# Performance work log

Measured on AMD Instinct MI355X. Metric: run time of the kernel, lower is better.

Reference implementation:

```python
import jax, jax.numpy as jnp
import numpy as np

D_MODEL = 1024
NUM_HEADS = 16
HEAD_DIM = D_MODEL // NUM_HEADS
ROPE_THETA = 10000.0


def apply_rope(x):
    # x: (B, H, S, d_k) interleaved-pair RoPE, angles pos / theta^(2i/d_k)
    S, d_k = x.shape[-2], x.shape[-1]
    inv_freq = ROPE_THETA ** (jnp.arange(0, d_k, 2, dtype=jnp.float32) / d_k)
    ang = jnp.arange(S, dtype=jnp.float32)[:, None] / inv_freq[None, :]  # (S, d_k/2)
    cos, sin = jnp.cos(ang), jnp.sin(ang)
    xp = x.reshape(x.shape[:-1] + (d_k // 2, 2))
    x0, x1 = xp[..., 0], xp[..., 1]
    out = jnp.stack([x0 * cos - x1 * sin, x0 * sin + x1 * cos], axis=-1)
    return out.reshape(x.shape)


def setup_inputs() -> dict:
    key = jax.random.key(0)
    k1, k2, k3 = jax.random.split(key, 3)
    B, S = 2, 2048
    std = 2.0 / (D_MODEL + 3 * D_MODEL)
    std_o = 2.0 / (D_MODEL + D_MODEL)
    return {
        "x": jax.random.normal(k1, (B, S, D_MODEL), dtype=jnp.float32),
        "W_qkv": jax.random.normal(k2, (3 * D_MODEL, D_MODEL), dtype=jnp.float32) * std,
        "W_o": jax.random.normal(k3, (D_MODEL, D_MODEL), dtype=jnp.float32) * std_o,
    }


def reference(x, W_qkv, W_o):
    B, S, d_model = x.shape
    H, d_k = NUM_HEADS, HEAD_DIM
    qkv = jnp.einsum('bsi,oi->bso', x, W_qkv)  # (B, S, 3*d_model)
    Q, K, V = jnp.split(qkv, 3, axis=-1)
    # (B, S, d_model) -> (B, H, S, d_k)
    def to_heads(t):
        return t.reshape(B, S, H, d_k).transpose(0, 2, 1, 3)
    Q, K, V = to_heads(Q), to_heads(K), to_heads(V)
    Q, K = apply_rope(Q), apply_rope(K)
    scores = jnp.einsum('bhqd,bhkd->bhqk', Q, K) / jnp.sqrt(jnp.float32(d_k))
    causal = jnp.tril(jnp.ones((S, S), dtype=bool))
    scores = jnp.where(causal, scores, -jnp.inf)
    attn = jax.nn.softmax(scores, axis=-1)
    out = jnp.einsum('bhqk,bhkd->bhqd', attn, V)
    out = out.transpose(0, 2, 1, 3).reshape(B, S, d_model)
    return jnp.einsum('bsi,oi->bso', out, W_o)
```

## Files before the change

kernel.cpp:

```cpp
#include <hip/hip_runtime.h>
#include <math.h>

#define kB 2
#define kS 2048
#define kD 1024
#define kH 16
#define kDk 64
#define kM (kB * kS)
#define kNT (kD / 64)
#define kLog2Theta 13.287712379549449
#define C_SCALE 0.18033688011112042f

typedef __attribute__((ext_vector_type(4))) float f32x4;
typedef __attribute__((ext_vector_type(16))) float f32x16;
typedef __attribute__((ext_vector_type(8))) __bf16 bf16x8;

__device__ __forceinline__ ushort f2bf(float f) {
  uint u = __float_as_uint(f);
  return (ushort)((u + 0x7fffu + ((u >> 16) & 1u)) >> 16);
}
__device__ __forceinline__ uint cvt_pk_bf16(float lo, float hi) {
  uint r;
  asm("v_cvt_pk_bf16_f32 %0, %1, %2" : "=v"(r) : "v"(lo), "v"(hi));
  return r;
}

typedef __attribute__((address_space(1))) void gvoid;
typedef __attribute__((address_space(3))) void lvoid;
__device__ __forceinline__ void load_lds16(const void* g, void* l) {
  __builtin_amdgcn_global_load_lds((gvoid*)g, (lvoid*)l, 16, 0, 0);
}

__global__ __launch_bounds__(256) void rope_table_kernel(float2* __restrict__ tab) {
  const int i = blockIdx.x * 256 + threadIdx.x;
  const int s = i >> 5, p = i & 31;
  const double ang = (double)s * exp2(-(double)p * (kLog2Theta / 32.0));
  tab[i] = make_float2((float)cos(ang), (float)sin(ang));
}

__global__ __launch_bounds__(256) void cast_all_kernel(
    const float* __restrict__ x, const float* __restrict__ wq,
    const float* __restrict__ wo, ushort* __restrict__ xb,
    ushort* __restrict__ wqb, ushort* __restrict__ wob) {
  const int i = blockIdx.x * 256 + threadIdx.x;
  const float* src;
  ushort* dst;
  int off;
  if (i < 1048576) {
    src = x; dst = xb; off = i;
  } else if (i < 1048576 + 786432) {
    src = wq; dst = wqb; off = i - 1048576;
  } else {
    src = wo; dst = wob; off = i - 1835008;
  }
  const float4 v = reinterpret_cast<const float4*>(src)[off];
  ushort4 o;
  o.x = f2bf(v.x); o.y = f2bf(v.y); o.z = f2bf(v.z); o.w = f2bf(v.w);
  reinterpret_cast<ushort4*>(dst)[off] = o;
}

__global__ __launch_bounds__(512) void qkv_mfma_kernel(
    const ushort* __restrict__ xb, const ushort* __restrict__ wqb,
    const float2* __restrict__ tab,
    ushort* __restrict__ q, ushort* __restrict__ k, ushort* __restrict__ vt) {
  __shared__ ushort As0[256 * 64], Bs0[256 * 64];
  __shared__ ushort As1[256 * 64], Bs1[256 * 64];
  const int tid = threadIdx.x;
  const int lane = tid & 63;
  const int wid = tid >> 6;
  const int wmi = wid >> 2, wni = wid & 3;
  const int fr = lane & 15, fq = lane >> 4;

  const int bid = blockIdx.x;
  const int xcd = bid & 7, li = bid >> 3;
  const int mt = ((xcd >> 1) << 2) + (li & 3);
  const int ntl = (xcd & 1) * 6 + (li >> 2);
  const int m0 = mt << 8, n0 = ntl << 8;

  f32x4 acc[8][4];
#pragma unroll
  for (int i = 0; i < 8; ++i)
#pragma unroll
    for (int j = 0; j < 4; ++j) acc[i][j] = {0.f, 0.f, 0.f, 0.f};

  auto stage = [&](int k0, ushort* Ad, ushort* Bd) {
#pragma unroll
    for (int u = 0; u < 4; ++u) {
      const int c = u * 512 + tid;
      const int r = c >> 3, sl = c & 7;
      const int col = k0 + ((sl ^ (r & 7)) << 3);
      load_lds16(&xb[(size_t)(m0 + r) * kD + col], &Ad[c << 3]);
      load_lds16(&wqb[(size_t)(n0 + r) * kD + col], &Bd[c << 3]);
    }
  };
  auto rdfrag = [&](const ushort* S, int row, int kk) -> bf16x8 {
    const int off = ((kk << 5) + (fq << 3)) ^ ((row & 7) << 3);
    return *reinterpret_cast<const bf16x8*>(&S[(row << 6) + off]);
  };

  stage(0, As0, Bs0);

  auto tile = [&](const ushort* cA, const ushort* cB, ushort* nA, ushort* nB,
                  bool pf, int k0n) {
    asm volatile("s_waitcnt vmcnt(0)" ::: "memory");
    __builtin_amdgcn_s_barrier();
    __builtin_amdgcn_sched_barrier(0);
#pragma unroll
    for (int kk = 0; kk < 2; ++kk) {
      bf16x8 af[8], bf_[4];
#pragma unroll
      for (int f = 0; f < 8; ++f)
        af[f] = rdfrag(cA, (wmi << 7) + f * 16 + fr, kk);
#pragma unroll
      for (int f = 0; f < 4; ++f)
        bf_[f] = rdfrag(cB, (wni << 6) + f * 16 + fr, kk);
      if (kk == 0 && pf) stage(k0n, nA, nB);
      asm volatile("s_waitcnt lgkmcnt(0)" ::: "memory");
      __builtin_amdgcn_sched_barrier(0);
      __builtin_amdgcn_s_setprio(1);
#pragma unroll
      for (int i = 0; i < 8; ++i)
#pragma unroll
        for (int j = 0; j < 4; ++j)
          acc[i][j] = __builtin_amdgcn_mfma_f32_16x16x32_bf16(
              af[i], bf_[j], acc[i][j], 0, 0, 0);
      __builtin_amdgcn_s_setprio(0);
    }
  };

  for (int t = 0; t < kNT; t += 2) {
    tile(As0, Bs0, As1, Bs1, true, (t + 1) << 6);
    tile(As1, Bs1, As0, Bs0, t + 2 < kNT, (t + 2) << 6);
  }

  const int tsel = n0 >> 10;
#pragma unroll
  for (int i = 0; i < 8; ++i) {
    const int mbase = m0 + (wmi << 7) + i * 16 + fq * 4;
    const int b = mbase >> 11, sbase = mbase & (kS - 1);
#pragma unroll
    for (int j = 0; j < 4; ++j) {
      const int n = n0 + (wni << 6) + j * 16 + fr;
      const int h = (n >> 6) & 15, d = n & 63;
      if (tsel == 2) {
        ushort4 o;
        o.x = f2bf(acc[i][j][0]);
        o.y = f2bf(acc[i][j][1]);
        o.z = f2bf(acc[i][j][2]);
        o.w = f2bf(acc[i][j][3]);
        *reinterpret_cast<ushort4*>(
            &vt[(((size_t)((b << 4) + h) << 6) + d) * kS + sbase]) = o;
      } else {
        ushort* dst = (tsel == 0) ? q : k;
#pragma unroll
        for (int r = 0; r < 4; ++r) {
          const int s = sbase + r;
          float val = acc[i][j][r];
          const float2 cs = tab[(s << 5) + (d >> 1)];
          const float partner = __shfl_xor(val, 1);
          val = (d & 1) ? (partner * cs.y + val * cs.x)
                        : (val * cs.x - partner * cs.y);
          if (tsel == 0) val *= C_SCALE;
          dst[(((size_t)((b << 4) + h) << 11) + s) * kDk + d] = f2bf(val);
        }
      }
    }
  }
}

__global__ __launch_bounds__(256) void proj_mfma_kernel(
    const ushort* __restrict__ ab, const ushort* __restrict__ wob,
    float* __restrict__ out) {
  __shared__ ushort As0[128 * 64], Bs0[128 * 64];
  __shared__ ushort As1[128 * 64], Bs1[128 * 64];
  const int tid = threadIdx.x;
  const int lane = tid & 63;
  const int wid = tid >> 6;
  const int wm = (wid >> 1) << 6, wn = (wid & 1) << 6;
  const int fr = lane & 15, fq = lane >> 4;

  const int bid = blockIdx.x;
  const int xcd = bid & 7, li = bid >> 3;
  const int mt = ((xcd >> 1) << 3) + (li & 7);
  const int ntl = ((xcd & 1) << 2) + (li >> 3);
  const int m0 = mt << 7, n0 = ntl << 7;

  f32x4 acc[4][4];
#pragma unroll
  for (int i = 0; i < 4; ++i)
#pragma unroll
    for (int j = 0; j < 4; ++j) acc[i][j] = {0.f, 0.f, 0.f, 0.f};

  auto stage = [&](int k0, ushort* Ad, ushort* Bd) {
#pragma unroll
    for (int u = 0; u < 4; ++u) {
      const int c = u * 256 + tid;
      const int r = c >> 3, sl = c & 7;
      const int col = k0 + ((sl ^ (r & 7)) << 3);
      load_lds16(&ab[(size_t)(m0 + r) * kD + col], &Ad[c << 3]);
      load_lds16(&wob[(size_t)(n0 + r) * kD + col], &Bd[c << 3]);
    }
  };
  auto rdfrag = [&](const ushort* S, int row, int kk) -> bf16x8 {
    const int off = ((kk << 5) + (fq << 3)) ^ ((row & 7) << 3);
    return *reinterpret_cast<const bf16x8*>(&S[(row << 6) + off]);
  };

  stage(0, As0, Bs0);

  auto tile = [&](const ushort* cA, const ushort* cB, ushort* nA, ushort* nB,
                  bool pf, int k0n) {
    asm volatile("s_waitcnt vmcnt(0)" ::: "memory");
    __builtin_amdgcn_s_barrier();
    __builtin_amdgcn_sched_barrier(0);
    bf16x8 af[2][4], bf_[2][4];
#pragma unroll
    for (int kk = 0; kk < 2; ++kk)
#pragma unroll
      for (int f = 0; f < 4; ++f) {
        af[kk][f]  = rdfrag(cA, wm + f * 16 + fr, kk);
        bf_[kk][f] = rdfrag(cB, wn + f * 16 + fr, kk);
      }
    if (pf) stage(k0n, nA, nB);
    asm volatile("s_waitcnt lgkmcnt(0)" ::: "memory");
    __builtin_amdgcn_sched_barrier(0);
    __builtin_amdgcn_s_setprio(1);
#pragma unroll
    for (int kk = 0; kk < 2; ++kk)
#pragma unroll
      for (int i = 0; i < 4; ++i)
#pragma unroll
        for (int j = 0; j < 4; ++j)
          acc[i][j] = __builtin_amdgcn_mfma_f32_16x16x32_bf16(
              af[kk][i], bf_[kk][j], acc[i][j], 0, 0, 0);
    __builtin_amdgcn_s_setprio(0);
  };

  for (int t = 0; t < kNT; t += 2) {
    tile(As0, Bs0, As1, Bs1, true, (t + 1) << 6);
    tile(As1, Bs1, As0, Bs0, t + 2 < kNT, (t + 2) << 6);
  }

#pragma unroll
  for (int i = 0; i < 4; ++i)
#pragma unroll
    for (int j = 0; j < 4; ++j)
#pragma unroll
      for (int r = 0; r < 4; ++r)
        out[(size_t)(m0 + wm + i * 16 + fq * 4 + r) * kD + n0 + wn + j * 16 + fr] =
            acc[i][j][r];
}

__global__ __launch_bounds__(256) void attn_mfma_kernel(
    const ushort* __restrict__ q, const ushort* __restrict__ k,
    const ushort* __restrict__ vt, ushort* __restrict__ ob) {
  __shared__ ushort smem[32768];
  const int tid = threadIdx.x;
  const int lane = tid & 63;
  const int wq = tid >> 6;
  const int l5 = lane >> 5;
  const int ln = lane & 31;
  const int swz = (ln & 7) << 4;

  const int bidx = blockIdx.x;
  const int xcd = bidx & 7, li = bidx >> 3;
  const int bh = (xcd << 2) + (li & 3);
  const int grp = li >> 2;
  const int qi = (grp < 8) ? (15 - grp) : (grp - 8);
  const int qb = qi << 7;
  const int nt = qi + 1;

  const ushort* qp = q + (size_t)bh * kS * kDk;
  const ushort* kp = k + (size_t)bh * kS * kDk;
  const ushort* vp = vt + (size_t)bh * kDk * kS;

  bf16x8 bq[4];
#pragma unroll
  for (int kk = 0; kk < 4; ++kk)
    bq[kk] = *reinterpret_cast<const bf16x8*>(
        &qp[(size_t)(qb + wq * 32 + ln) * kDk + kk * 16 + l5 * 8]);

  f32x16 acc_o[2];
#pragma unroll
  for (int db = 0; db < 2; ++db)
#pragma unroll
    for (int r = 0; r < 16; ++r) acc_o[db][r] = 0.f;
  float l_run = 0.f;

  auto stage = [&](int kt, int buf) {
    ushort* Kd = smem + buf * 16384;
    ushort* Vd = Kd + 8192;
#pragma unroll
    for (int u = 0; u < 4; ++u) {
      const int c = u * 256 + tid;
      {
        const int r = c >> 3, sl = c & 7;
        load_lds16(&kp[(size_t)(kt * 128 + r) * kDk + ((sl ^ (r & 7)) << 3)],
                   &Kd[c << 3]);
      }
      {
        const int r = c >> 4, sl = c & 15;
        load_lds16(&vp[(size_t)r * kS + kt * 128 + ((sl ^ (r & 7)) << 3)],
                   &Vd[c << 3]);
      }
    }
  };

  stage(0, 0);

  for (int kt = 0; kt < nt; ++kt) {
    const int cur = kt & 1;
    __syncthreads();
    if (kt + 1 < nt) stage(kt + 1, cur ^ 1);

    const char* KsB = reinterpret_cast<const char*>(smem + cur * 16384);
    const char* VtsB = KsB + 16384;

    f32x16 accs[4];
    __builtin_amdgcn_s_setprio(1);
#pragma unroll
    for (int cb = 0; cb < 4; ++cb) {
#pragma unroll
      for (int r = 0; r < 16; ++r) accs[cb][r] = 0.f;
#pragma unroll
      for (int kk = 0; kk < 4; ++kk) {
        const bf16x8 av = *reinterpret_cast<const bf16x8*>(
            KsB + (cb * 32 + ln) * 128 + ((kk * 32 + l5 * 16) ^ swz));
        accs[cb] = __builtin_amdgcn_mfma_f32_32x32x16_bf16(av, bq[kk], accs[cb], 0, 0, 0);
      }
    }
    __builtin_amdgcn_s_setprio(0);

    if (kt == qi) {
      const int lim = (wq << 5) + ln;
#pragma unroll
      for (int cb = 0; cb < 4; ++cb)
#pragma unroll
        for (int r = 0; r < 16; ++r) {
          const int key = cb * 32 + (r & 3) + 8 * (r >> 2) + 4 * l5;
          if (key > lim) accs[cb][r] = -INFINITY;
        }
    }

    uint c8[4][8];
    float lsum = 0.f;
#pragma unroll
    for (int cb = 0; cb < 4; ++cb) {
      float s0 = 0.f, s1 = 0.f, s2 = 0.f, s3 = 0.f;
      float p[16];
#pragma unroll
      for (int r = 0; r < 16; ++r) {
        p[r] = exp2f(accs[cb][r]);
        if ((r & 3) == 0) s0 += p[r];
        else if ((r & 3) == 1) s1 += p[r];
        else if ((r & 3) == 2) s2 += p[r];
        else s3 += p[r];
      }
      lsum += (s0 + s1) + (s2 + s3);
#pragma unroll
      for (int t = 0; t < 8; ++t)
        c8[cb][t] = cvt_pk_bf16(p[2 * t], p[2 * t + 1]);
    }
    l_run += lsum;

    __builtin_amdgcn_s_setprio(1);
#pragma unroll
    for (int kb = 0; kb < 8; ++kb) {
      const int cb = kb >> 1, base = (kb & 1) * 4;
      const uint a0 = c8[cb][base + 0], a1 = c8[cb][base + 1];
      const uint b0 = c8[cb][base + 2], b1 = c8[cb][base + 3];
      const uint sa0 = (uint)__shfl_xor((int)a0, 32);
      const uint sa1 = (uint)__shfl_xor((int)a1, 32);
      const uint sb0 = (uint)__shfl_xor((int)b0, 32);
      const uint sb1 = (uint)__shfl_xor((int)b1, 32);
      uint4 dw;
      dw.x = l5 ? sb0 : a0;
      dw.y = l5 ? sb1 : a1;
      dw.z = l5 ? b0 : sa0;
      dw.w = l5 ? b1 : sa1;
      const bf16x8 pa = *reinterpret_cast<const bf16x8*>(&dw);
#pragma unroll
      for (int db = 0; db < 2; ++db) {
        const bf16x8 av = *reinterpret_cast<const bf16x8*>(
            VtsB + (db * 32 + ln) * 256 + ((kb * 32 + l5 * 16) ^ swz));
        acc_o[db] = __builtin_amdgcn_mfma_f32_32x32x16_bf16(av, pa, acc_o[db], 0, 0, 0);
      }
    }
    __builtin_amdgcn_s_setprio(0);
  }

  const float l_tot = l_run + __shfl_xor(l_run, 32);
  const float linv = 1.f / l_tot;

  __syncthreads();
  char* OsB = reinterpret_cast<char*>(smem);
  const int orow = wq * 32 + ln;
#pragma unroll
  for (int db = 0; db < 2; ++db)
#pragma unroll
    for (int t = 0; t < 8; ++t) {
      const int reg = 2 * t;
      const int d = db * 32 + (reg & 3) + 8 * (reg >> 2) + 4 * l5;
      const uint pk2 = cvt_pk_bf16(acc_o[db][reg] * linv, acc_o[db][reg + 1] * linv);
      *reinterpret_cast<uint*>(OsB + orow * 128 + ((d * 2) ^ swz)) = pk2;
    }
  __syncthreads();
  const int b = bh >> 4, h = bh & 15;
  const int qrw = tid >> 1, half = tid & 1;
  ushort* orow_g = ob + ((size_t)(b * kS + qb + qrw)) * kD + h * kDk + half * 32;
#pragma unroll
  for (int sl = 0; sl < 4; ++sl) {
    const uint4 vdat = *reinterpret_cast<const uint4*>(
        OsB + qrw * 128 + ((half * 64 + sl * 16) ^ ((qrw & 7) << 4)));
    *reinterpret_cast<uint4*>(orow_g + sl * 8) = vdat;
  }
}

extern "C" void kernel_launch(void* const* d_in, const int* in_sizes, int n_in,
                              void* d_out, int out_size, void* d_ws,
                              size_t ws_size, hipStream_t stream) {
  const float* x = (const float*)d_in[0];
  const float* wqkv = (const float*)d_in[1];
  const float* wo = (const float*)d_in[2];
  float* out = (float*)d_out;
  char* w = (char*)d_ws;
  const size_t MB = 1024 * 1024;
  ushort* qb  = (ushort*)(w + 0 * MB);
  ushort* kb  = (ushort*)(w + 8 * MB);
  ushort* vtb = (ushort*)(w + 16 * MB);
  ushort* xb  = (ushort*)(w + 24 * MB);
  ushort* wqb = (ushort*)(w + 32 * MB);
  ushort* wob = (ushort*)(w + 38 * MB);
  float2* tab = (float2*)(w + 40 * MB);
  ushort* attnb = xb;

  hipLaunchKernelGGL(rope_table_kernel, dim3(256), dim3(256), 0, stream, tab);
  hipLaunchKernelGGL(cast_all_kernel, dim3(8192), dim3(256), 0, stream,
                     x, wqkv, wo, xb, wqb, wob);
  hipLaunchKernelGGL(qkv_mfma_kernel, dim3(192), dim3(512), 0, stream,
                     xb, wqb, tab, qb, kb, vtb);
  hipLaunchKernelGGL(attn_mfma_kernel, dim3(512), dim3(256), 0, stream,
                     qb, kb, vtb, attnb);
  hipLaunchKernelGGL(proj_mfma_kernel, dim3(256), dim3(256), 0, stream,
                     attnb, wob, out);
}
```

Baseline: 146.8 us.

## Merge setup kernels, shrink QKV tiles, read K/V directly from global in attention

Folds the RoPE table and cast kernels into one launch to save a kernel launch. Changes the QKV GEMM from 256x256 tiles with 512 threads to 128x128 tiles with 256 threads, raising the block count from 192 to 768 for better CU occupancy. The attention kernel drops LDS staging of K and V and loads MFMA fragments straight from global memory. That relies on the cache for reuse and gives up the double-buffered prefetch, so memory latency may become exposed.

```diff
diff --git a/kernel.cpp b/kernel.cpp
--- a/kernel.cpp
+++ b/kernel.cpp
@@ -31,62 +31,64 @@
   __builtin_amdgcn_global_load_lds((gvoid*)g, (lvoid*)l, 16, 0, 0);
 }
 
-__global__ __launch_bounds__(256) void rope_table_kernel(float2* __restrict__ tab) {
-  const int i = blockIdx.x * 256 + threadIdx.x;
-  const int s = i >> 5, p = i & 31;
-  const double ang = (double)s * exp2(-(double)p * (kLog2Theta / 32.0));
-  tab[i] = make_float2((float)cos(ang), (float)sin(ang));
-}
-
-__global__ __launch_bounds__(256) void cast_all_kernel(
+__global__ __launch_bounds__(256) void setup_kernel(
     const float* __restrict__ x, const float* __restrict__ wq,
     const float* __restrict__ wo, ushort* __restrict__ xb,
-    ushort* __restrict__ wqb, ushort* __restrict__ wob) {
-  const int i = blockIdx.x * 256 + threadIdx.x;
-  const float* src;
-  ushort* dst;
-  int off;
-  if (i < 1048576) {
-    src = x; dst = xb; off = i;
-  } else if (i < 1048576 + 786432) {
-    src = wq; dst = wqb; off = i - 1048576;
+    ushort* __restrict__ wqb, ushort* __restrict__ wob,
+    float2* __restrict__ tab) {
+  const int bid = blockIdx.x;
+  if (bid < 8192) {
+    const int i = bid * 256 + threadIdx.x;
+    const float* src;
+    ushort* dst;
+    int off;
+    if (i < 1048576) {
+      src = x; dst = xb; off = i;
+    } else if (i < 1048576 + 786432) {
+      src = wq; dst = wqb; off = i - 1048576;
+    } else {
+      src = wo; dst = wob; off = i - 1835008;
+    }
+    const float4 v = reinterpret_cast<const float4*>(src)[off];
+    ushort4 o;
+    o.x = f2bf(v.x); o.y = f2bf(v.y); o.z = f2bf(v.z); o.w = f2bf(v.w);
+    reinterpret_cast<ushort4*>(dst)[off] = o;
   } else {
-    src = wo; dst = wob; off = i - 1835008;
-  }
-  const float4 v = reinterpret_cast<const float4*>(src)[off];
-  ushort4 o;
-  o.x = f2bf(v.x); o.y = f2bf(v.y); o.z = f2bf(v.z); o.w = f2bf(v.w);
-  reinterpret_cast<ushort4*>(dst)[off] = o;
-}
-
-__global__ __launch_bounds__(512) void qkv_mfma_kernel(
+    const int i = (bid - 8192) * 256 + threadIdx.x;
+    const int s = i >> 5, p = i & 31;
+    const double ang = (double)s * exp2(-(double)p * (kLog2Theta / 32.0));
+    tab[i] = make_float2((float)cos(ang), (float)sin(ang));
+  }
+}
+
+__global__ __launch_bounds__(256) void qkv_mfma_kernel(
     const ushort* __restrict__ xb, const ushort* __restrict__ wqb,
     const float2* __restrict__ tab,
     ushort* __restrict__ q, ushort* __restrict__ k, ushort* __restrict__ vt) {
-  __shared__ ushort As0[256 * 64], Bs0[256 * 64];
-  __shared__ ushort As1[256 * 64], Bs1[256 * 64];
+  __shared__ ushort As0[128 * 64], Bs0[128 * 64];
+  __shared__ ushort As1[128 * 64], Bs1[128 * 64];
   const int tid = threadIdx.x;
   const int lane = tid & 63;
   const int wid = tid >> 6;
-  const int wmi = wid >> 2, wni = wid & 3;
+  const int wm = (wid >> 1) << 6, wn = (wid & 1) << 6;
   const int fr = lane & 15, fq = lane >> 4;
 
   const int bid = blockIdx.x;
   const int xcd = bid & 7, li = bid >> 3;
-  const int mt = ((xcd >> 1) << 2) + (li & 3);
-  const int ntl = (xcd & 1) * 6 + (li >> 2);
-  const int m0 = mt << 8, n0 = ntl << 8;
-
-  f32x4 acc[8][4];
-#pragma unroll
-  for (int i = 0; i < 8; ++i)
+  const int nt = xcd * 3 + (li % 3);
+  const int mt = li / 3;
+  const int m0 = mt << 7, n0 = nt << 7;
+
+  f32x4 acc[4][4];
+#pragma unroll
+  for (int i = 0; i < 4; ++i)
 #pragma unroll
     for (int j = 0; j < 4; ++j) acc[i][j] = {0.f, 0.f, 0.f, 0.f};
 
   auto stage = [&](int k0, ushort* Ad, ushort* Bd) {
 #pragma unroll
     for (int u = 0; u < 4; ++u) {
-      const int c = u * 512 + tid;
+      const int c = u * 256 + tid;
       const int r = c >> 3, sl = c & 7;
       const int col = k0 + ((sl ^ (r & 7)) << 3);
       load_lds16(&xb[(size_t)(m0 + r) * kD + col], &Ad[c << 3]);
@@ -105,27 +107,27 @@
     asm volatile("s_waitcnt vmcnt(0)" ::: "memory");
     __builtin_amdgcn_s_barrier();
     __builtin_amdgcn_sched_barrier(0);
-#pragma unroll
-    for (int kk = 0; kk < 2; ++kk) {
-      bf16x8 af[8], bf_[4];
-#pragma unroll
-      for (int f = 0; f < 8; ++f)
-        af[f] = rdfrag(cA, (wmi << 7) + f * 16 + fr, kk);
-#pragma unroll
-      for (int f = 0; f < 4; ++f)
-        bf_[f] = rdfrag(cB, (wni << 6) + f * 16 + fr, kk);
-      if (kk == 0 && pf) stage(k0n, nA, nB);
-      asm volatile("s_waitcnt lgkmcnt(0)" ::: "memory");
-      __builtin_amdgcn_sched_barrier(0);
-      __builtin_amdgcn_s_setprio(1);
-#pragma unroll
-      for (int i = 0; i < 8; ++i)
+    bf16x8 af[2][4], bf_[2][4];
+#pragma unroll
+    for (int kk = 0; kk < 2; ++kk)
+#pragma unroll
+      for (int f = 0; f < 4; ++f) {
+        af[kk][f]  = rdfrag(cA, wm + f * 16 + fr, kk);
+        bf_[kk][f] = rdfrag(cB, wn + f * 16 + fr, kk);
+      }
+    if (pf) stage(k0n, nA, nB);
+    asm volatile("s_waitcnt lgkmcnt(0)" ::: "memory");
+    __builtin_amdgcn_sched_barrier(0);
+    __builtin_amdgcn_s_setprio(1);
+#pragma unroll
+    for (int kk = 0; kk < 2; ++kk)
+#pragma unroll
+      for (int i = 0; i < 4; ++i)
 #pragma unroll
         for (int j = 0; j < 4; ++j)
           acc[i][j] = __builtin_amdgcn_mfma_f32_16x16x32_bf16(
-              af[i], bf_[j], acc[i][j], 0, 0, 0);
-      __builtin_amdgcn_s_setprio(0);
-    }
+              af[kk][i], bf_[kk][j], acc[i][j], 0, 0, 0);
+    __builtin_amdgcn_s_setprio(0);
   };
 
   for (int t = 0; t < kNT; t += 2) {
@@ -135,12 +137,12 @@
 
   const int tsel = n0 >> 10;
 #pragma unroll
-  for (int i = 0; i < 8; ++i) {
-    const int mbase = m0 + (wmi << 7) + i * 16 + fq * 4;
+  for (int i = 0; i < 4; ++i) {
+    const int mbase = m0 + wm + i * 16 + fq * 4;
     const int b = mbase >> 11, sbase = mbase & (kS - 1);
 #pragma unroll
     for (int j = 0; j < 4; ++j) {
-      const int n = n0 + (wni << 6) + j * 16 + fr;
+      const int n = n0 + wn + j * 16 + fr;
       const int h = (n >> 6) & 15, d = n & 63;
       if (tsel == 2) {
         ushort4 o;
@@ -254,7 +256,7 @@
 __global__ __launch_bounds__(256) void attn_mfma_kernel(
     const ushort* __restrict__ q, const ushort* __restrict__ k,
     const ushort* __restrict__ vt, ushort* __restrict__ ob) {
-  __shared__ ushort smem[32768];
+  __shared__ ushort smem[8192];
   const int tid = threadIdx.x;
   const int lane = tid & 63;
   const int wq = tid >> 6;
@@ -287,35 +289,7 @@
     for (int r = 0; r < 16; ++r) acc_o[db][r] = 0.f;
   float l_run = 0.f;
 
-  auto stage = [&](int kt, int buf) {
-    ushort* Kd = smem + buf * 16384;
-    ushort* Vd = Kd + 8192;
-#pragma unroll
-    for (int u = 0; u < 4; ++u) {
-      const int c = u * 256 + tid;
-      {
-        const int r = c >> 3, sl = c & 7;
-        load_lds16(&kp[(size_t)(kt * 128 + r) * kDk + ((sl ^ (r & 7)) << 3)],
-                   &Kd[c << 3]);
-      }
-      {
-        const int r = c >> 4, sl = c & 15;
-        load_lds16(&vp[(size_t)r * kS + kt * 128 + ((sl ^ (r & 7)) << 3)],
-                   &Vd[c << 3]);
-      }
-    }
-  };
-
-  stage(0, 0);
-
   for (int kt = 0; kt < nt; ++kt) {
-    const int cur = kt & 1;
-    __syncthreads();
-    if (kt + 1 < nt) stage(kt + 1, cur ^ 1);
-
-    const char* KsB = reinterpret_cast<const char*>(smem + cur * 16384);
-    const char* VtsB = KsB + 16384;
-
     f32x16 accs[4];
     __builtin_amdgcn_s_setprio(1);
 #pragma unroll
@@ -325,7 +299,7 @@
 #pragma unroll
       for (int kk = 0; kk < 4; ++kk) {
         const bf16x8 av = *reinterpret_cast<const bf16x8*>(
-            KsB + (cb * 32 + ln) * 128 + ((kk * 32 + l5 * 16) ^ swz));
+            &kp[(size_t)(kt * 128 + cb * 32 + ln) * kDk + kk * 16 + l5 * 8]);
         accs[cb] = __builtin_amdgcn_mfma_f32_32x32x16_bf16(av, bq[kk], accs[cb], 0, 0, 0);
       }
     }
@@ -382,7 +356,7 @@
 #pragma unroll
       for (int db = 0; db < 2; ++db) {
         const bf16x8 av = *reinterpret_cast<const bf16x8*>(
-            VtsB + (db * 32 + ln) * 256 + ((kb * 32 + l5 * 16) ^ swz));
+            &vp[(size_t)(db * 32 + ln) * kS + kt * 128 + kb * 16 + l5 * 8]);
         acc_o[db] = __builtin_amdgcn_mfma_f32_32x32x16_bf16(av, pa, acc_o[db], 0, 0, 0);
       }
     }
@@ -434,10 +408,9 @@
   float2* tab = (float2*)(w + 40 * MB);
   ushort* attnb = xb;
 
-  hipLaunchKernelGGL(rope_table_kernel, dim3(256), dim3(256), 0, stream, tab);
-  hipLaunchKernelGGL(cast_all_kernel, dim3(8192), dim3(256), 0, stream,
-                     x, wqkv, wo, xb, wqb, wob);
-  hipLaunchKernelGGL(qkv_mfma_kernel, dim3(192), dim3(512), 0, stream,
+  hipLaunchKernelGGL(setup_kernel, dim3(8448), dim3(256), 0, stream,
+                     x, wqkv, wo, xb, wqb, wob, tab);
+  hipLaunchKernelGGL(qkv_mfma_kernel, dim3(768), dim3(256), 0, stream,
                      xb, wqb, tab, qb, kb, vtb);
   hipLaunchKernelGGL(attn_mfma_kernel, dim3(512), dim3(256), 0, stream,
                      qb, kb, vtb, attnb);
```

New measurement: 161.2 us. 9.8% more time.
